# Performance work log

Measured on AMD Instinct MI355X. Metric: run time of the kernel, lower is better.

## Reference

```python
import jax, jax.numpy as jnp
import numpy as np

EMBED = 384
HEADS = 6
HEAD_SIZE = EMBED // HEADS
EPS = 1e-5


def _layernorm(x, g, b):
    mu = jnp.mean(x, axis=-1, keepdims=True)
    var = jnp.mean(jnp.square(x - mu), axis=-1, keepdims=True)
    return (x - mu) * jax.lax.rsqrt(var + EPS) * g + b


def setup_inputs() -> dict:
    key = jax.random.key(0)
    ks = jax.random.split(key, 16)
    B, T = 64, 256
    s_in = 1.0 / np.sqrt(EMBED)
    return {
        "x": jax.random.normal(ks[0], (B, T, EMBED), dtype=jnp.float32),
        # per-head q/k/v projections, stacked over heads: [H, C, D]
        "Wq": jax.random.normal(ks[1], (HEADS, EMBED, HEAD_SIZE), dtype=jnp.float32) * s_in,
        "bq": jnp.zeros((HEADS, HEAD_SIZE), dtype=jnp.float32),
        "Wk": jax.random.normal(ks[2], (HEADS, EMBED, HEAD_SIZE), dtype=jnp.float32) * s_in,
        "bk": jnp.zeros((HEADS, HEAD_SIZE), dtype=jnp.float32),
        "Wv": jax.random.normal(ks[3], (HEADS, EMBED, HEAD_SIZE), dtype=jnp.float32) * s_in,
        "bv": jnp.zeros((HEADS, HEAD_SIZE), dtype=jnp.float32),
        "Wp": jax.random.normal(ks[4], (EMBED, EMBED), dtype=jnp.float32) * s_in,
        "bp": jnp.zeros((EMBED,), dtype=jnp.float32),
        "W1": jax.random.normal(ks[5], (EMBED, EMBED), dtype=jnp.float32) * s_in,
        "b1": jnp.zeros((EMBED,), dtype=jnp.float32),
        "W2": jax.random.normal(ks[6], (EMBED, EMBED), dtype=jnp.float32) * s_in,
        "b2": jnp.zeros((EMBED,), dtype=jnp.float32),
        "ln1_g": jnp.ones((EMBED,), dtype=jnp.float32),
        "ln1_b": jnp.zeros((EMBED,), dtype=jnp.float32),
        "ln2_g": jnp.ones((EMBED,), dtype=jnp.float32),
        "ln2_b": jnp.zeros((EMBED,), dtype=jnp.float32),
    }


def reference(x, Wq, bq, Wk, bk, Wv, bv, Wp, bp, W1, b1, W2, b2,
              ln1_g, ln1_b, ln2_g, ln2_b):
    B, T, C = x.shape
    h = _layernorm(x, ln1_g, ln1_b)
    # batched per-head projections: [B,H,T,D]
    q = jnp.einsum('btc,hcd->bhtd', h, Wq) + bq[None, :, None, :]
    k = jnp.einsum('btc,hcd->bhtd', h, Wk) + bk[None, :, None, :]
    v = jnp.einsum('btc,hcd->bhtd', h, Wv) + bv[None, :, None, :]
    # NOTE: original scales by embed_size**0.5 (C=384), not head_size.
    wei = jnp.einsum('bhtd,bhsd->bhts', q, k) / jnp.sqrt(jnp.float32(C))
    causal = jnp.tril(jnp.ones((T, T), dtype=bool))
    wei = jnp.where(causal[None, None], wei, -jnp.inf)
    wei = jax.nn.softmax(wei, axis=-1)  # dropout = identity in eval
    attn = jnp.einsum('bhts,bhsd->bhtd', wei, v)  # [B,H,T,D]
    # concat heads in head order -> [B,T,C]
    attn = attn.transpose(0, 2, 1, 3).reshape(B, T, C)
    x = x + attn @ Wp + bp
    h2 = _layernorm(x, ln2_g, ln2_b)
    ff = jax.nn.relu(h2 @ W1 + b1) @ W2 + b2
    return x + ff
```

## Files before the change

### kernel.cpp

```cpp
#include <hip/hip_runtime.h>

typedef _Float16 f16;
typedef _Float16 half8 __attribute__((ext_vector_type(8)));
typedef _Float16 half4v __attribute__((ext_vector_type(4)));
typedef float floatx4 __attribute__((ext_vector_type(4)));

#define B_ 64
#define T_ 256
#define C_ 384
#define H_ 6
#define D_ 64
#define NROWS (B_*T_)

typedef __attribute__((address_space(3))) void lds_void_t;
typedef const __attribute__((address_space(1))) void gvoid_t;

__device__ __forceinline__ void g2lds16(const void* g, void* l) {
  __builtin_amdgcn_global_load_lds((gvoid_t*)g, (lds_void_t*)l, 16, 0, 0);
}

__global__ __launch_bounds__(256) void prep_ln_kernel(
    const float* __restrict__ Wq, const float* __restrict__ Wk, const float* __restrict__ Wv,
    const float* __restrict__ bq, const float* __restrict__ bk, const float* __restrict__ bv,
    const float* __restrict__ Wp, const float* __restrict__ W1, const float* __restrict__ W2,
    f16* __restrict__ Wqkv_t, f16* __restrict__ Wp_t, f16* __restrict__ W1_t, f16* __restrict__ W2_t,
    float* __restrict__ bqkv,
    const float* __restrict__ x, const float* __restrict__ gamma, const float* __restrict__ beta,
    f16* __restrict__ hout)
{
  const int bid = blockIdx.x;
  const int tid = threadIdx.x;
  if (bid >= 217) {
    int row = (bid - 217) * 4 + (tid >> 6);
    int lane = tid & 63;
    const float* xr = x + (size_t)row * 384;
    float v[6]; float s = 0.f;
#pragma unroll
    for (int j = 0; j < 6; j++) { v[j] = xr[lane + 64*j]; s += v[j]; }
#pragma unroll
    for (int m = 1; m < 64; m <<= 1) s += __shfl_xor(s, m);
    float mu = s * (1.f/384.f);
    float var = 0.f;
#pragma unroll
    for (int j = 0; j < 6; j++) { float d = v[j]-mu; var += d*d; }
#pragma unroll
    for (int m = 1; m < 64; m <<= 1) var += __shfl_xor(var, m);
    float rs = rsqrtf(var * (1.f/384.f) + 1e-5f);
    f16* orow = hout + (size_t)row*384;
#pragma unroll
    for (int j = 0; j < 6; j++) {
      int col = lane + 64*j;
      orow[col] = (f16)((v[j]-mu)*rs*gamma[col] + beta[col]);
    }
    return;
  }
  if (bid == 216) {
    for (int i = tid; i < 1152; i += 256) {
      float v;
      if (i < 384)      v = bq[i];
      else if (i < 768) v = bk[i - 384];
      else              v = bv[i - 768];
      bqkv[i] = v;
    }
    return;
  }
  __shared__ __align__(16) float tile[64*68];
  const float* src; int srcStride; f16* dst;
  if (bid < 108) {
    int mat = bid / 36, rem = bid - mat*36;
    int h = rem / 6, kt = rem - h*6;
    const float* W = (mat == 0) ? Wq : (mat == 1) ? Wk : Wv;
    src = W + (size_t)(h*384 + kt*64)*64;
    srcStride = 64;
    dst = Wqkv_t + (size_t)(mat*384 + h*64)*384 + kt*64;
  } else {
    int b2 = bid - 108;
    int mat = b2 / 36, rem = b2 - mat*36;
    int kt = rem / 6, ct = rem - kt*6;
    const float* W = (mat == 0) ? Wp : (mat == 1) ? W1 : W2;
    src = W + (size_t)(kt*64)*384 + ct*64;
    srcStride = 384;
    f16* O = (mat == 0) ? Wp_t : (mat == 1) ? W1_t : W2_t;
    dst = O + (size_t)(ct*64)*384 + kt*64;
  }
#pragma unroll
  for (int i = 0; i < 4; i++) {
    int idx = i*256 + tid;
    int r = idx >> 4, c4 = idx & 15;
    float4 v = *(const float4*)(src + (size_t)r*srcStride + c4*4);
    *(float4*)(&tile[r*68 + c4*4]) = v;
  }
  __syncthreads();
#pragma unroll
  for (int i = 0; i < 4; i++) {
    int idx = i*256 + tid;
    int d = idx >> 4, k4 = idx & 15;
    half4v o;
#pragma unroll
    for (int j = 0; j < 4; j++) o[j] = (f16)tile[(k4*4 + j)*68 + d];
    *(half4v*)(dst + (size_t)d*384 + k4*4) = o;
  }
}

__global__ __launch_bounds__(256) void ln_kernel(const float* __restrict__ x,
    const float* __restrict__ gamma, const float* __restrict__ beta, f16* __restrict__ out)
{
  int row = blockIdx.x * 4 + (threadIdx.x >> 6);
  int lane = threadIdx.x & 63;
  const float* xr = x + (size_t)row * 384;
  float v[6]; float s = 0.f;
#pragma unroll
  for (int j = 0; j < 6; j++) { v[j] = xr[lane + 64*j]; s += v[j]; }
#pragma unroll
  for (int m = 1; m < 64; m <<= 1) s += __shfl_xor(s, m);
  float mu = s * (1.f/384.f);
  float var = 0.f;
#pragma unroll
  for (int j = 0; j < 6; j++) { float d = v[j]-mu; var += d*d; }
#pragma unroll
  for (int m = 1; m < 64; m <<= 1) var += __shfl_xor(var, m);
  float rs = rsqrtf(var * (1.f/384.f) + 1e-5f);
  f16* orow = out + (size_t)row*384;
#pragma unroll
  for (int j = 0; j < 6; j++) {
    int col = lane + 64*j;
    orow[col] = (f16)((v[j]-mu)*rs*gamma[col] + beta[col]);
  }
}

template<int MODE>
__global__ __launch_bounds__(256) void gemm_kernel(
    const f16* __restrict__ A, const f16* __restrict__ Bt,
    const float* __restrict__ bias, const float* __restrict__ res,
    void* __restrict__ outp, int ldo)
{
  __shared__ __align__(16) f16 As[2][128*32];
  __shared__ __align__(16) f16 Bs[2][128*32];
  const int tid = threadIdx.x;
  const int lane = tid & 63, w = tid >> 6;
  const int wm = w >> 1, wn = w & 1;
  const int q = lane >> 4, c15 = lane & 15;
  const long row0 = (long)blockIdx.x * 128;
  const long col0 = (long)blockIdx.y * 128;
  floatx4 acc[4][4] = {};

  const int c0 = tid,        r0c = c0 >> 2, p0 = c0 & 3, g0 = p0 ^ ((r0c >> 1) & 3);
  const int c1 = 256 + tid,  r1c = c1 >> 2, p1 = c1 & 3, g1 = p1 ^ ((r1c >> 1) & 3);
  const f16* Arow0 = A  + (row0 + r0c)*384 + g0*8;
  const f16* Arow1 = A  + (row0 + r1c)*384 + g1*8;
  const f16* Brow0 = Bt + (col0 + r0c)*384 + g0*8;
  const f16* Brow1 = Bt + (col0 + r1c)*384 + g1*8;
  const int dof0 = (w*64)*8, dof1 = (256 + w*64)*8;

#define GEMM_STAGE(buf, kk) do { \
    g2lds16(Arow0 + (kk), &As[buf][dof0]); \
    g2lds16(Arow1 + (kk), &As[buf][dof1]); \
    g2lds16(Brow0 + (kk), &Bs[buf][dof0]); \
    g2lds16(Brow1 + (kk), &Bs[buf][dof1]); \
  } while (0)

#define GEMM_COMPUTE(buf) do { \
    half8 af[4], bf[4]; \
    _Pragma("unroll") \
    for (int mi = 0; mi < 4; mi++) { \
      int r = wm*64 + mi*16 + c15; \
      int ph = q ^ ((r >> 1) & 3); \
      af[mi] = *(const half8*)(&As[buf][r*32 + ph*8]); \
    } \
    _Pragma("unroll") \
    for (int ni = 0; ni < 4; ni++) { \
      int r = wn*64 + ni*16 + c15; \
      int ph = q ^ ((r >> 1) & 3); \
      bf[ni] = *(const half8*)(&Bs[buf][r*32 + ph*8]); \
    } \
    _Pragma("unroll") \
    for (int mi = 0; mi < 4; mi++) \
      _Pragma("unroll") \
      for (int ni = 0; ni < 4; ni++) \
        acc[mi][ni] = __builtin_amdgcn_mfma_f32_16x16x32_f16(af[mi], bf[ni], acc[mi][ni], 0, 0, 0); \
  } while (0)

  GEMM_STAGE(0, 0);
  __syncthreads();
#pragma unroll
  for (int t = 0; t < 11; ++t) {
    GEMM_STAGE((t + 1) & 1, (t + 1) * 32);
    GEMM_COMPUTE(t & 1);
    __syncthreads();
  }
  GEMM_COMPUTE(1);

#undef GEMM_STAGE
#undef GEMM_COMPUTE

#pragma unroll
  for (int ni = 0; ni < 4; ni++) {
    long col = col0 + wn*64 + ni*16 + c15;
    float bv = bias[col];
#pragma unroll
    for (int mi = 0; mi < 4; mi++) {
      long rowb = row0 + wm*64 + mi*16 + q*4;
#pragma unroll
      for (int r = 0; r < 4; r++) {
        float vo = acc[mi][ni][r] + bv;
        if (MODE == 1) vo = vo > 0.f ? vo : 0.f;
        long o = (rowb + r) * (long)ldo + col;
        if (MODE == 2) {
          ((float*)outp)[o] = vo + res[o];
        } else {
          ((f16*)outp)[o] = (f16)vo;
        }
      }
    }
  }
}

__global__ __launch_bounds__(256, 4) void attn_kernel(const f16* __restrict__ qkv,
                                                      f16* __restrict__ attn_out)
{
  __shared__ __align__(16) char kvbuf[32768];
  __shared__ __align__(16) f16 Pbuf[4][16*64];
  f16* Ks = (f16*)kvbuf;
  unsigned int* vTw = (unsigned int*)kvbuf;
  f16* vT = (f16*)kvbuf;

  const int tid = threadIdx.x;
  const int bid = blockIdx.x;
  const int bh = bid >> 2, qt = bid & 3;
  const int b = bh / 6, h = bh - b*6;
  const f16* qp = qkv + (size_t)b*256*1152 + h*64;
  const f16* kp = qp + 384;
  const f16* vp = qp + 768;
  const int lane = tid & 63, w = tid >> 6;
  const int q = lane >> 4, c15 = lane & 15;

  {
    const int iters = (qt + 1) * 2;
    const int pcbase = w*64 + lane;
    for (int i = 0; i < iters; i++) {
      int pc = i*256 + pcbase;
      int rc = pc >> 3, p = pc & 7;
      int c = p ^ (rc & 7);
      g2lds16(kp + (size_t)rc*1152 + c*8, (char*)kvbuf + (size_t)(i*256 + w*64)*16);
    }
  }

  const int nmax = qt*4 + w;
  const int trow0 = qt*64 + w*16;
  const f16* qrow = qp + (size_t)(trow0 + c15)*1152 + q*8;
  half8 aq0 = *(const half8*)(qrow);
  half8 aq1 = *(const half8*)(qrow + 32);

  __syncthreads();

  floatx4 sacc[16];
  __builtin_amdgcn_s_setprio(1);
#pragma unroll
  for (int ni = 0; ni < 16; ni++) {
    if (ni <= nmax) {
      int s = ni*16 + c15;
      const f16* kr = Ks + s*64;
      int p0 = q ^ (s & 7);
      half8 b0 = *(const half8*)(kr + p0*8);
      half8 b1 = *(const half8*)(kr + (p0 ^ 4)*8);
      floatx4 a = {0.f, 0.f, 0.f, 0.f};
      a = __builtin_amdgcn_mfma_f32_16x16x32_f16(aq0, b0, a, 0, 0, 0);
      a = __builtin_amdgcn_mfma_f32_16x16x32_f16(aq1, b1, a, 0, 0, 0);
      sacc[ni] = a;
    }
  }
  __builtin_amdgcn_s_setprio(0);
  __syncthreads();

  half8 va[4], vb[4];
#pragma unroll
  for (int i = 0; i < 4; i++) {
    if (i <= qt) {
      int idx = i*256 + tid;
      int sp = idx >> 3, part = idx & 7;
      const f16* v0 = vp + (size_t)(2*sp)*1152 + part*8;
      va[i] = *(const half8*)(v0);
      vb[i] = *(const half8*)(v0 + 1152);
    }
  }

  const float scale = 0.051031036307982884f;
  float mx[4] = {-1e30f, -1e30f, -1e30f, -1e30f};
#pragma unroll
  for (int ni = 0; ni < 16; ni++) {
    if (ni < nmax) {
#pragma unroll
      for (int r = 0; r < 4; r++) { float v = sacc[ni][r]*scale; sacc[ni][r] = v; mx[r] = fmaxf(mx[r], v); }
    } else if (ni == nmax) {
#pragma unroll
      for (int r = 0; r < 4; r++) {
        float v = sacc[ni][r]*scale;
        v = (c15 <= q*4 + r) ? v : -1e30f;
        sacc[ni][r] = v; mx[r] = fmaxf(mx[r], v);
      }
    }
  }
#pragma unroll
  for (int r = 0; r < 4; r++) {
    mx[r] = fmaxf(mx[r], __shfl_xor(mx[r], 1));
    mx[r] = fmaxf(mx[r], __shfl_xor(mx[r], 2));
    mx[r] = fmaxf(mx[r], __shfl_xor(mx[r], 4));
    mx[r] = fmaxf(mx[r], __shfl_xor(mx[r], 8));
  }
  float l[4] = {0.f, 0.f, 0.f, 0.f};
#pragma unroll
  for (int ni = 0; ni < 16; ni++) {
    if (ni <= nmax) {
#pragma unroll
      for (int r = 0; r < 4; r++) { float p = __expf(sacc[ni][r] - mx[r]); sacc[ni][r] = p; l[r] += p; }
    }
  }
#pragma unroll
  for (int r = 0; r < 4; r++) {
    l[r] += __shfl_xor(l[r], 1);
    l[r] += __shfl_xor(l[r], 2);
    l[r] += __shfl_xor(l[r], 4);
    l[r] += __shfl_xor(l[r], 8);
  }

#pragma unroll
  for (int i = 0; i < 4; i++) {
    if (i <= qt) {
      int idx = i*256 + tid;
      int sp = idx >> 3, part = idx & 7;
      int csp = sp >> 2, spw = sp & 3;
#pragma unroll
      for (int j = 0; j < 8; j++) {
        int d = part*8 + j;
        int swz = (d & 15) ^ (d >> 3);
        int p = csp ^ swz;
        union { struct { f16 lo, hi; } s; unsigned int u; } pk;
        pk.s.lo = va[i][j]; pk.s.hi = vb[i][j];
        vTw[d*128 + p*4 + spw] = pk.u;
      }
    }
  }
  __syncthreads();

  f16* Pw = &Pbuf[w][0];
  floatx4 oacc[4] = {};
  const int kend_w = (nmax + 1) * 16;
#pragma unroll
  for (int ch = 0; ch < 4; ch++) {
    if (ch*64 < kend_w) {
#pragma unroll
      for (int nl = 0; nl < 4; nl++) {
        int ni = ch*4 + nl;
        if (ni <= nmax) {
#pragma unroll
          for (int r = 0; r < 4; r++) {
            int row = q*4 + r;
            int colp = nl*16 + c15;
            int php = (colp >> 3) ^ (row & 7);
            Pw[row*64 + php*8 + (colp & 7)] = (f16)sacc[ni][r];
          }
        } else if (ni == nmax + 1) {
#pragma unroll
          for (int r = 0; r < 4; r++) {
            int row = q*4 + r;
            int colp = nl*16 + c15;
            int php = (colp >> 3) ^ (row & 7);
            Pw[row*64 + php*8 + (colp & 7)] = (f16)0.f;
          }
        }
      }
      __builtin_amdgcn_s_setprio(1);
#pragma unroll
      for (int kc = 0; kc < 2; kc++) {
        if (ch*64 + kc*32 < kend_w) {
          int pc = (kc*4 + q) ^ (c15 & 7);
          half8 ap = *(const half8*)(Pw + c15*64 + pc*8);
          int sc = ch*8 + kc*4 + q;
#pragma unroll
          for (int nt = 0; nt < 4; nt++) {
            int d = nt*16 + c15;
            int swz = (d & 15) ^ (d >> 3);
            half8 bv = *(const half8*)(vT + d*256 + ((sc ^ swz))*8);
            oacc[nt] = __builtin_amdgcn_mfma_f32_16x16x32_f16(ap, bv, oacc[nt], 0, 0, 0);
          }
        }
      }
      __builtin_amdgcn_s_setprio(0);
    }
  }

  float rl[4];
#pragma unroll
  for (int r = 0; r < 4; r++) rl[r] = 1.0f / l[r];
#pragma unroll
  for (int nt = 0; nt < 4; nt++) {
#pragma unroll
    for (int r = 0; r < 4; r++) {
      int t = trow0 + q*4 + r;
      int d = nt*16 + c15;
      attn_out[(size_t)(b*256 + t)*384 + h*64 + d] = (f16)(oacc[nt][r] * rl[r]);
    }
  }
}

extern "C" void kernel_launch(void* const* d_in, const int* in_sizes, int n_in,
                              void* d_out, int out_size, void* d_ws, size_t ws_size,
                              hipStream_t stream) {
  const float* x   = (const float*)d_in[0];
  const float* Wq  = (const float*)d_in[1];
  const float* bq  = (const float*)d_in[2];
  const float* Wk  = (const float*)d_in[3];
  const float* bk  = (const float*)d_in[4];
  const float* Wv  = (const float*)d_in[5];
  const float* bv  = (const float*)d_in[6];
  const float* Wp  = (const float*)d_in[7];
  const float* bp  = (const float*)d_in[8];
  const float* W1  = (const float*)d_in[9];
  const float* b1  = (const float*)d_in[10];
  const float* W2  = (const float*)d_in[11];
  const float* b2  = (const float*)d_in[12];
  const float* g1  = (const float*)d_in[13];
  const float* be1 = (const float*)d_in[14];
  const float* g2  = (const float*)d_in[15];
  const float* be2 = (const float*)d_in[16];

  char* ws = (char*)d_ws;
  size_t off = 0;
  auto alloc = [&](size_t bytes) -> void* {
    void* p = ws + off;
    off += (bytes + 255) & ~(size_t)255;
    return p;
  };
  f16*   Wqkv_t = (f16*)  alloc(1152*384*sizeof(f16));
  f16*   Wp_t   = (f16*)  alloc(384*384*sizeof(f16));
  f16*   W1_t   = (f16*)  alloc(384*384*sizeof(f16));
  f16*   W2_t   = (f16*)  alloc(384*384*sizeof(f16));
  float* bqkv   = (float*)alloc(1152*sizeof(float));
  f16*   h      = (f16*)  alloc((size_t)NROWS*384*sizeof(f16));
  f16*   qkv    = (f16*)  alloc((size_t)NROWS*1152*sizeof(f16));
  f16*   attnb  = (f16*)  alloc((size_t)NROWS*384*sizeof(f16));
  float* x2     = (float*)alloc((size_t)NROWS*384*sizeof(float));
  f16*   h2     = (f16*)  alloc((size_t)NROWS*384*sizeof(f16));
  f16*   mid    = (f16*)  alloc((size_t)NROWS*384*sizeof(f16));

  prep_ln_kernel<<<217 + NROWS/4, 256, 0, stream>>>(Wq, Wk, Wv, bq, bk, bv, Wp, W1, W2,
                                                    Wqkv_t, Wp_t, W1_t, W2_t, bqkv,
                                                    x, g1, be1, h);
  gemm_kernel<0><<<dim3(128, 9), 256, 0, stream>>>(h, Wqkv_t, bqkv, nullptr, qkv, 1152);
  attn_kernel<<<B_*H_*4, 256, 0, stream>>>(qkv, attnb);
  gemm_kernel<2><<<dim3(128, 3), 256, 0, stream>>>(attnb, Wp_t, bp, x, x2, 384);
  ln_kernel<<<NROWS/4, 256, 0, stream>>>(x2, g2, be2, h2);
  gemm_kernel<1><<<dim3(128, 3), 256, 0, stream>>>(h2, W1_t, b1, nullptr, mid, 384);
  gemm_kernel<2><<<dim3(128, 3), 256, 0, stream>>>(mid, W2_t, b2, x2, (float*)d_out, 384);
}
```

Baseline: 206.8 us.

## Fuse projection with LayerNorm2 and fuse both FFN GEMMs in one kernel

Replaces the separate output-projection GEMM and LayerNorm kernel with one kernel. Each 32-row block computes all 384 columns, adds the residual and applies LayerNorm in-block. The two FFN GEMMs are also merged, keeping the ReLU intermediate in LDS so it is never written to global memory. This removes two launches and the global round trips for the x2 re-read and the mid buffer. In exchange, each block re-streams the full weight matrix for only 32 rows and computes variance in a single pass (E[x²]−mu²), which is less numerically robust.

```diff
diff --git a/kernel.cpp b/kernel.cpp
--- a/kernel.cpp
+++ b/kernel.cpp
@@ -102,37 +102,9 @@
   }
 }
 
-__global__ __launch_bounds__(256) void ln_kernel(const float* __restrict__ x,
-    const float* __restrict__ gamma, const float* __restrict__ beta, f16* __restrict__ out)
-{
-  int row = blockIdx.x * 4 + (threadIdx.x >> 6);
-  int lane = threadIdx.x & 63;
-  const float* xr = x + (size_t)row * 384;
-  float v[6]; float s = 0.f;
-#pragma unroll
-  for (int j = 0; j < 6; j++) { v[j] = xr[lane + 64*j]; s += v[j]; }
-#pragma unroll
-  for (int m = 1; m < 64; m <<= 1) s += __shfl_xor(s, m);
-  float mu = s * (1.f/384.f);
-  float var = 0.f;
-#pragma unroll
-  for (int j = 0; j < 6; j++) { float d = v[j]-mu; var += d*d; }
-#pragma unroll
-  for (int m = 1; m < 64; m <<= 1) var += __shfl_xor(var, m);
-  float rs = rsqrtf(var * (1.f/384.f) + 1e-5f);
-  f16* orow = out + (size_t)row*384;
-#pragma unroll
-  for (int j = 0; j < 6; j++) {
-    int col = lane + 64*j;
-    orow[col] = (f16)((v[j]-mu)*rs*gamma[col] + beta[col]);
-  }
-}
-
-template<int MODE>
-__global__ __launch_bounds__(256) void gemm_kernel(
+__global__ __launch_bounds__(256) void gemm_qkv_kernel(
     const f16* __restrict__ A, const f16* __restrict__ Bt,
-    const float* __restrict__ bias, const float* __restrict__ res,
-    void* __restrict__ outp, int ldo)
+    const float* __restrict__ bias, f16* __restrict__ outp, int ldo)
 {
   __shared__ __align__(16) f16 As[2][128*32];
   __shared__ __align__(16) f16 Bs[2][128*32];
@@ -203,13 +175,298 @@
 #pragma unroll
       for (int r = 0; r < 4; r++) {
         float vo = acc[mi][ni][r] + bv;
-        if (MODE == 1) vo = vo > 0.f ? vo : 0.f;
-        long o = (rowb + r) * (long)ldo + col;
-        if (MODE == 2) {
-          ((float*)outp)[o] = vo + res[o];
-        } else {
-          ((f16*)outp)[o] = (f16)vo;
+        outp[(rowb + r) * (long)ldo + col] = (f16)vo;
+      }
+    }
+  }
+}
+
+__global__ __launch_bounds__(384) void projln_kernel(
+    const f16* __restrict__ A, const f16* __restrict__ Bt,
+    const float* __restrict__ bias, const float* __restrict__ x,
+    const float* __restrict__ g2, const float* __restrict__ be2,
+    float* __restrict__ x2, f16* __restrict__ h2)
+{
+  __shared__ __align__(16) f16 As[2][32*32];
+  __shared__ __align__(16) f16 Bs[2][384*32];
+  __shared__ float lnred[2][32][8];
+  __shared__ float lnmv[2][32];
+  const int tid = threadIdx.x;
+  const int lane = tid & 63, w = tid >> 6;
+  const int q = lane >> 4, c15 = lane & 15;
+  const long row0 = (long)blockIdx.x * 32;
+  floatx4 acc[2][4] = {};
+
+  const int ca = w*64 + lane;
+  const int rcA = ca >> 2, pA = ca & 3, gA = pA ^ ((rcA >> 1) & 3);
+  const f16* srcA = A + (row0 + rcA)*384 + gA*8;
+  long offB[4];
+#pragma unroll
+  for (int i = 0; i < 4; i++) {
+    int cb = (i*6 + w)*64 + lane;
+    int rcB = cb >> 2, pB = cb & 3, gB = pB ^ ((rcB >> 1) & 3);
+    offB[i] = (long)rcB*384 + gB*8;
+  }
+
+#define PL_STAGE(buf, kk) do { \
+    if (w < 2) g2lds16(srcA + (kk), &As[buf][w*512]); \
+    _Pragma("unroll") \
+    for (int i = 0; i < 4; i++) \
+      g2lds16(Bt + offB[i] + (kk), &Bs[buf][(i*6 + w)*512]); \
+  } while (0)
+
+#define PL_COMPUTE(buf) do { \
+    half8 af[2], bf[4]; \
+    _Pragma("unroll") \
+    for (int mi = 0; mi < 2; mi++) { \
+      int r = mi*16 + c15; \
+      int ph = q ^ ((r >> 1) & 3); \
+      af[mi] = *(const half8*)(&As[buf][r*32 + ph*8]); \
+    } \
+    _Pragma("unroll") \
+    for (int ni = 0; ni < 4; ni++) { \
+      int rb = w*64 + ni*16 + c15; \
+      int phb = q ^ ((rb >> 1) & 3); \
+      bf[ni] = *(const half8*)(&Bs[buf][rb*32 + phb*8]); \
+    } \
+    _Pragma("unroll") \
+    for (int mi = 0; mi < 2; mi++) \
+      _Pragma("unroll") \
+      for (int ni = 0; ni < 4; ni++) \
+        acc[mi][ni] = __builtin_amdgcn_mfma_f32_16x16x32_f16(af[mi], bf[ni], acc[mi][ni], 0, 0, 0); \
+  } while (0)
+
+  PL_STAGE(0, 0);
+  __syncthreads();
+#pragma unroll
+  for (int t = 0; t < 11; ++t) {
+    PL_STAGE((t + 1) & 1, (t + 1) * 32);
+    PL_COMPUTE(t & 1);
+    __syncthreads();
+  }
+  PL_COMPUTE(1);
+
+#undef PL_STAGE
+#undef PL_COMPUTE
+
+  float colb[4];
+#pragma unroll
+  for (int ni = 0; ni < 4; ni++) colb[ni] = bias[w*64 + ni*16 + c15];
+  float vals[2][4][4];
+#pragma unroll
+  for (int mi = 0; mi < 2; mi++) {
+#pragma unroll
+    for (int rr = 0; rr < 4; rr++) {
+      long row = row0 + mi*16 + q*4 + rr;
+#pragma unroll
+      for (int ni = 0; ni < 4; ni++) {
+        long col = w*64 + ni*16 + c15;
+        float v = acc[mi][ni][rr] + colb[ni] + x[row*384 + col];
+        vals[mi][ni][rr] = v;
+        x2[row*384 + col] = v;
+      }
+    }
+  }
+#pragma unroll
+  for (int mi = 0; mi < 2; mi++) {
+#pragma unroll
+    for (int rr = 0; rr < 4; rr++) {
+      float s = 0.f, s2 = 0.f;
+#pragma unroll
+      for (int ni = 0; ni < 4; ni++) { float v = vals[mi][ni][rr]; s += v; s2 += v*v; }
+      s  += __shfl_xor(s, 1);  s  += __shfl_xor(s, 2);  s  += __shfl_xor(s, 4);  s  += __shfl_xor(s, 8);
+      s2 += __shfl_xor(s2, 1); s2 += __shfl_xor(s2, 2); s2 += __shfl_xor(s2, 4); s2 += __shfl_xor(s2, 8);
+      if (c15 == 0) {
+        int lr = mi*16 + q*4 + rr;
+        lnred[0][lr][w] = s;
+        lnred[1][lr][w] = s2;
+      }
+    }
+  }
+  __syncthreads();
+  if (tid < 32) {
+    float s = 0.f, s2 = 0.f;
+#pragma unroll
+    for (int j = 0; j < 6; j++) { s += lnred[0][tid][j]; s2 += lnred[1][tid][j]; }
+    float mu = s * (1.f/384.f);
+    float var = s2 * (1.f/384.f) - mu*mu;
+    lnmv[0][tid] = mu;
+    lnmv[1][tid] = rsqrtf(var + 1e-5f);
+  }
+  __syncthreads();
+  float cg[4], cb2[4];
+#pragma unroll
+  for (int ni = 0; ni < 4; ni++) {
+    int col = w*64 + ni*16 + c15;
+    cg[ni] = g2[col]; cb2[ni] = be2[col];
+  }
+#pragma unroll
+  for (int mi = 0; mi < 2; mi++) {
+#pragma unroll
+    for (int rr = 0; rr < 4; rr++) {
+      int lr = mi*16 + q*4 + rr;
+      float mu = lnmv[0][lr], rs = lnmv[1][lr];
+      long row = row0 + lr;
+#pragma unroll
+      for (int ni = 0; ni < 4; ni++) {
+        long col = w*64 + ni*16 + c15;
+        h2[row*384 + col] = (f16)((vals[mi][ni][rr] - mu)*rs*cg[ni] + cb2[ni]);
+      }
+    }
+  }
+}
+
+__global__ __launch_bounds__(384) void ffn_kernel(
+    const f16* __restrict__ A, const f16* __restrict__ B1t, const f16* __restrict__ B2t,
+    const float* __restrict__ b1, const float* __restrict__ b2,
+    const float* __restrict__ x2, float* __restrict__ out)
+{
+  __shared__ __align__(16) f16 As[2][32*32];
+  __shared__ __align__(16) f16 Bs[2][384*32];
+  __shared__ __align__(16) f16 midb[12][32*32];
+  const int tid = threadIdx.x;
+  const int lane = tid & 63, w = tid >> 6;
+  const int q = lane >> 4, c15 = lane & 15;
+  const long row0 = (long)blockIdx.x * 32;
+  floatx4 acc[2][4] = {};
+
+  const int ca = w*64 + lane;
+  const int rcA = ca >> 2, pA = ca & 3, gA = pA ^ ((rcA >> 1) & 3);
+  const f16* srcA = A + (row0 + rcA)*384 + gA*8;
+  long offB[4];
+#pragma unroll
+  for (int i = 0; i < 4; i++) {
+    int cb = (i*6 + w)*64 + lane;
+    int rcB = cb >> 2, pB = cb & 3, gB = pB ^ ((rcB >> 1) & 3);
+    offB[i] = (long)rcB*384 + gB*8;
+  }
+
+#define FF_STAGE(buf, kk, BT, WITH_A) do { \
+    if (WITH_A && w < 2) g2lds16(srcA + (kk), &As[buf][w*512]); \
+    _Pragma("unroll") \
+    for (int i = 0; i < 4; i++) \
+      g2lds16(BT + offB[i] + (kk), &Bs[buf][(i*6 + w)*512]); \
+  } while (0)
+
+#define FF_COMPUTE(buf) do { \
+    half8 af[2], bf[4]; \
+    _Pragma("unroll") \
+    for (int mi = 0; mi < 2; mi++) { \
+      int r = mi*16 + c15; \
+      int ph = q ^ ((r >> 1) & 3); \
+      af[mi] = *(const half8*)(&As[buf][r*32 + ph*8]); \
+    } \
+    _Pragma("unroll") \
+    for (int ni = 0; ni < 4; ni++) { \
+      int rb = w*64 + ni*16 + c15; \
+      int phb = q ^ ((rb >> 1) & 3); \
+      bf[ni] = *(const half8*)(&Bs[buf][rb*32 + phb*8]); \
+    } \
+    _Pragma("unroll") \
+    for (int mi = 0; mi < 2; mi++) \
+      _Pragma("unroll") \
+      for (int ni = 0; ni < 4; ni++) \
+        acc[mi][ni] = __builtin_amdgcn_mfma_f32_16x16x32_f16(af[mi], bf[ni], acc[mi][ni], 0, 0, 0); \
+  } while (0)
+
+#define FF_COMPUTE2(buf, t) do { \
+    half8 af[2], bf[4]; \
+    _Pragma("unroll") \
+    for (int mi = 0; mi < 2; mi++) { \
+      int r = mi*16 + c15; \
+      int ph = q ^ ((r >> 1) & 3); \
+      af[mi] = *(const half8*)(&midb[t][r*32 + ph*8]); \
+    } \
+    _Pragma("unroll") \
+    for (int ni = 0; ni < 4; ni++) { \
+      int rb = w*64 + ni*16 + c15; \
+      int phb = q ^ ((rb >> 1) & 3); \
+      bf[ni] = *(const half8*)(&Bs[buf][rb*32 + phb*8]); \
+    } \
+    _Pragma("unroll") \
+    for (int mi = 0; mi < 2; mi++) \
+      _Pragma("unroll") \
+      for (int ni = 0; ni < 4; ni++) \
+        acc[mi][ni] = __builtin_amdgcn_mfma_f32_16x16x32_f16(af[mi], bf[ni], acc[mi][ni], 0, 0, 0); \
+  } while (0)
+
+  FF_STAGE(0, 0, B1t, 1);
+  __syncthreads();
+#pragma unroll
+  for (int t = 0; t < 11; ++t) {
+    FF_STAGE((t + 1) & 1, (t + 1) * 32, B1t, 1);
+    FF_COMPUTE(t & 1);
+    __syncthreads();
+  }
+  FF_COMPUTE(1);
+
+  {
+    float colb[4];
+#pragma unroll
+    for (int ni = 0; ni < 4; ni++) colb[ni] = b1[w*64 + ni*16 + c15];
+#pragma unroll
+    for (int mi = 0; mi < 2; mi++) {
+#pragma unroll
+      for (int rr = 0; rr < 4; rr++) {
+        int lr = mi*16 + q*4 + rr;
+        int s = (lr >> 1) & 3;
+#pragma unroll
+        for (int ni = 0; ni < 4; ni++) {
+          int cc = w*64 + ni*16 + c15;
+          float v = acc[mi][ni][rr] + colb[ni];
+          v = v > 0.f ? v : 0.f;
+          int chunk = cc >> 5;
+          int kk = cc & 31;
+          int pos = ((kk >> 3) ^ s)*8 + (kk & 7);
+          midb[chunk][lr*32 + pos] = (f16)v;
         }
+      }
+    }
+  }
+#pragma unroll
+  for (int mi = 0; mi < 2; mi++)
+#pragma unroll
+    for (int ni = 0; ni < 4; ni++)
+      acc[mi][ni] = floatx4{0.f, 0.f, 0.f, 0.f};
+
+  FF_STAGE(0, 0, B2t, 0);
+  __syncthreads();
+
+  float vres[2][4][4];
+#pragma unroll
+  for (int mi = 0; mi < 2; mi++)
+#pragma unroll
+    for (int rr = 0; rr < 4; rr++) {
+      long row = row0 + mi*16 + q*4 + rr;
+#pragma unroll
+      for (int ni = 0; ni < 4; ni++)
+        vres[mi][ni][rr] = x2[row*384 + w*64 + ni*16 + c15];
+    }
+  float colb2[4];
+#pragma unroll
+  for (int ni = 0; ni < 4; ni++) colb2[ni] = b2[w*64 + ni*16 + c15];
+
+#pragma unroll
+  for (int t = 0; t < 11; ++t) {
+    FF_STAGE((t + 1) & 1, (t + 1) * 32, B2t, 0);
+    FF_COMPUTE2(t & 1, t);
+    __syncthreads();
+  }
+  FF_COMPUTE2(1, 11);
+
+#undef FF_STAGE
+#undef FF_COMPUTE
+#undef FF_COMPUTE2
+
+#pragma unroll
+  for (int mi = 0; mi < 2; mi++) {
+#pragma unroll
+    for (int rr = 0; rr < 4; rr++) {
+      long row = row0 + mi*16 + q*4 + rr;
+#pragma unroll
+      for (int ni = 0; ni < 4; ni++) {
+        long col = w*64 + ni*16 + c15;
+        out[row*384 + col] = acc[mi][ni][rr] + colb2[ni] + vres[mi][ni][rr];
       }
     }
   }
@@ -441,15 +698,12 @@
   f16*   attnb  = (f16*)  alloc((size_t)NROWS*384*sizeof(f16));
   float* x2     = (float*)alloc((size_t)NROWS*384*sizeof(float));
   f16*   h2     = (f16*)  alloc((size_t)NROWS*384*sizeof(f16));
-  f16*   mid    = (f16*)  alloc((size_t)NROWS*384*sizeof(f16));
 
   prep_ln_kernel<<<217 + NROWS/4, 256, 0, stream>>>(Wq, Wk, Wv, bq, bk, bv, Wp, W1, W2,
                                                     Wqkv_t, Wp_t, W1_t, W2_t, bqkv,
                                                     x, g1, be1, h);
-  gemm_kernel<0><<<dim3(128, 9), 256, 0, stream>>>(h, Wqkv_t, bqkv, nullptr, qkv, 1152);
+  gemm_qkv_kernel<<<dim3(128, 9), 256, 0, stream>>>(h, Wqkv_t, bqkv, qkv, 1152);
   attn_kernel<<<B_*H_*4, 256, 0, stream>>>(qkv, attnb);
-  gemm_kernel<2><<<dim3(128, 3), 256, 0, stream>>>(attnb, Wp_t, bp, x, x2, 384);
-  ln_kernel<<<NROWS/4, 256, 0, stream>>>(x2, g2, be2, h2);
-  gemm_kernel<1><<<dim3(128, 3), 256, 0, stream>>>(h2, W1_t, b1, nullptr, mid, 384);
-  gemm_kernel<2><<<dim3(128, 3), 256, 0, stream>>>(mid, W2_t, b2, x2, (float*)d_out, 384);
+  projln_kernel<<<NROWS/32, 384, 0, stream>>>(attnb, Wp_t, bp, x, g2, be2, x2, h2);
+  ffn_kernel<<<NROWS/32, 384, 0, stream>>>(h2, W1_t, W2_t, b1, b2, x2, (float*)d_out);
 }
```

Result: slower. 228.5 us (+10.5%).
